# Kernel tuning notes

Hardware: AMD Instinct MI355X
Metric: run time of the kernel (lower is better)

Reference implementation:

```python
import jax, jax.numpy as jnp
import numpy as np

DIM = 1024
HID = 2732  # int(2*4*1024/3) rounded up to multiple of 4
E = 8
TOPK = 2
B, S = 2, 2048


def setup_inputs() -> dict:
    key = jax.random.key(0)
    ks = jax.random.split(key, 5)
    scale = 0.02
    return {
        "x": jax.random.normal(ks[0], (B, S, DIM), dtype=jnp.float32),
        "Wg": jax.random.normal(ks[1], (E, DIM), dtype=jnp.float32) * scale,
        "W1": jax.random.normal(ks[2], (E, HID, DIM), dtype=jnp.float32) * scale,
        "W2": jax.random.normal(ks[3], (E, DIM, HID), dtype=jnp.float32) * scale,
        "W3": jax.random.normal(ks[4], (E, HID, DIM), dtype=jnp.float32) * scale,
    }


def reference(x, Wg, W1, W2, W3):
    b, s, d = x.shape
    xt = x.reshape(b * s, d)                              # [N, d]
    scores = xt @ Wg.T                                    # [N, E]
    w, idx = jax.lax.top_k(scores, TOPK)                  # [N, k]
    w = jax.nn.softmax(w, axis=-1)
    n = xt.shape[0]
    # combine weights scattered back into [N, E] (top-k indices are distinct per row)
    cw = jnp.zeros((n, E), dtype=x.dtype).at[jnp.arange(n)[:, None], idx].set(w)
    # dense per-expert SwiGLU (mathematically identical to masked dispatch)
    h1 = jnp.einsum('nd,ehd->neh', xt, W1)                # [N, E, H]
    h3 = jnp.einsum('nd,ehd->neh', xt, W3)
    h = jax.nn.silu(h1) * h3
    y = jnp.einsum('neh,edh->ned', h, W2)                 # [N, E, d]
    out = jnp.einsum('ned,ne->nd', y, cw)                 # [N, d]
    return out
```

## Files before the change

kernel.cpp:

```cpp
#include <hip/hip_runtime.h>
#include <hip/hip_bf16.h>
#include <stdint.h>

#define DIM   1024
#define HID   2732
#define HPAD  2816
#define NEXP  8
#define NTOK  4096
#define NROW  8192

typedef __attribute__((ext_vector_type(8))) short bf16x8;
typedef __attribute__((ext_vector_type(4))) float f32x4;

__device__ __forceinline__ unsigned short f2bf(float f) {
    union { float f; uint32_t u; } v; v.f = f;
    uint32_t u = v.u;
    return (unsigned short)((u + 0x7FFFu + ((u >> 16) & 1u)) >> 16);
}

#define ASYNC_CP16(g, l) __builtin_amdgcn_global_load_lds( \
    (const __attribute__((address_space(1))) void*)(g), \
    (__attribute__((address_space(3))) void*)(l), 16, 0, 0)

__global__ void conv_w13_kernel(const float* __restrict__ src,
                                unsigned short* __restrict__ dst) {
    size_t t = (size_t)blockIdx.x * 256 + threadIdx.x;
    int d4 = (int)(t & 255);
    size_t rest = t >> 8;
    int hp = (int)(rest % HPAD);
    int e  = (int)(rest / HPAD);
    ushort4 o;
    if (hp < HID) {
        float4 v = *(const float4*)(src + ((size_t)e * HID + hp) * DIM + d4 * 4);
        o.x = f2bf(v.x); o.y = f2bf(v.y); o.z = f2bf(v.z); o.w = f2bf(v.w);
    } else {
        o.x = o.y = o.z = o.w = 0;
    }
    *(ushort4*)(dst + t * 4) = o;
}

__global__ void conv_w2_kernel(const float* __restrict__ src,
                               unsigned short* __restrict__ dst) {
    size_t t = (size_t)blockIdx.x * 256 + threadIdx.x;
    int h4 = (int)(t % (HPAD / 4));
    size_t rest = t / (HPAD / 4);
    int d = (int)(rest % DIM);
    int e = (int)(rest / DIM);
    ushort4 o;
    if (h4 * 4 < HID) {
        float4 v = *(const float4*)(src + ((size_t)e * DIM + d) * HID + h4 * 4);
        o.x = f2bf(v.x); o.y = f2bf(v.y); o.z = f2bf(v.z); o.w = f2bf(v.w);
    } else {
        o.x = o.y = o.z = o.w = 0;
    }
    *(ushort4*)(dst + t * 4) = o;
}

__global__ void route_kernel(const float* __restrict__ x, const float* __restrict__ Wg,
                             int* __restrict__ counts, int* __restrict__ a_exp,
                             int* __restrict__ a_rank, float* __restrict__ a_w) {
    int wave = threadIdx.x >> 6, lane = threadIdx.x & 63;
    int n = blockIdx.x * 4 + wave;
    const float* xr = x + (size_t)n * DIM + lane * 16;
    float p[NEXP];
#pragma unroll
    for (int e = 0; e < NEXP; ++e) p[e] = 0.f;
#pragma unroll
    for (int i = 0; i < 4; ++i) {
        float4 xv = *(const float4*)(xr + i * 4);
#pragma unroll
        for (int e = 0; e < NEXP; ++e) {
            float4 wv = *(const float4*)(Wg + e * DIM + lane * 16 + i * 4);
            p[e] += xv.x * wv.x + xv.y * wv.y + xv.z * wv.z + xv.w * wv.w;
        }
    }
#pragma unroll
    for (int off = 32; off > 0; off >>= 1)
#pragma unroll
        for (int e = 0; e < NEXP; ++e) p[e] += __shfl_xor(p[e], off);
    if (lane == 0) {
        int i1 = -1, i2 = -1; float m1 = -1e30f, m2 = -1e30f;
#pragma unroll
        for (int e = 0; e < NEXP; ++e) {
            float s = p[e];
            if (s > m1) { m2 = m1; i2 = i1; m1 = s; i1 = e; }
            else if (s > m2) { m2 = s; i2 = e; }
        }
        float e2 = __expf(m2 - m1);
        float inv = 1.f / (1.f + e2);
        int a = n * 2;
        a_exp[a] = i1;  a_w[a] = inv;        a_rank[a] = atomicAdd(&counts[i1], 1);
        a_exp[a+1] = i2; a_w[a+1] = e2 * inv; a_rank[a+1] = atomicAdd(&counts[i2], 1);
    }
}

__global__ void scan_kernel(const int* __restrict__ counts, int* __restrict__ offsets) {
    if (threadIdx.x == 0) {
        int s = 0;
        for (int e = 0; e < NEXP; ++e) { offsets[e] = s; s += counts[e]; }
    }
}

__global__ void gather_kernel(const float* __restrict__ x, const int* __restrict__ a_exp,
                              const int* __restrict__ a_rank, const float* __restrict__ a_w,
                              const int* __restrict__ offsets,
                              unsigned short* __restrict__ XG,
                              int* __restrict__ tok_of_row, float* __restrict__ wgt_of_row) {
    int a = blockIdx.x, n = a >> 1;
    int row = offsets[a_exp[a]] + a_rank[a];
    if (threadIdx.x == 0) { tok_of_row[row] = n; wgt_of_row[row] = a_w[a]; }
    float4 xv = *(const float4*)(x + (size_t)n * DIM + threadIdx.x * 4);
    ushort4 o; o.x = f2bf(xv.x); o.y = f2bf(xv.y); o.z = f2bf(xv.z); o.w = f2bf(xv.w);
    *(ushort4*)(XG + (size_t)row * DIM + threadIdx.x * 4) = o;
}

__global__ __launch_bounds__(256, 2) void gemm1_kernel(
    const unsigned short* __restrict__ XG,
    const unsigned short* __restrict__ W1b,
    const unsigned short* __restrict__ W3b,
    const int* __restrict__ counts, const int* __restrict__ offsets,
    unsigned short* __restrict__ Hbuf)
{
    const int e = blockIdx.z, mtile = blockIdx.y, ntile = blockIdx.x;
    const int cnt = counts[e];
    if (mtile * 128 >= cnt) return;
    const int rowstart = offsets[e] + mtile * 128;

    __shared__ __align__(16) unsigned short As[128 * 64];
    __shared__ __align__(16) unsigned short B1s[64 * 64];
    __shared__ __align__(16) unsigned short B3s[64 * 64];

    const int tid = threadIdx.x, lane = tid & 63, wave = tid >> 6;
    const int wm = wave >> 1, wn = wave & 1;
    const int quad = lane >> 4;

    const unsigned short* w1e = W1b + (size_t)e * HPAD * DIM;
    const unsigned short* w3e = W3b + (size_t)e * HPAD * DIM;

    const int srow = tid >> 3, scol = (tid & 7) * 8;
    const unsigned short* ag[4];
#pragma unroll
    for (int r = 0; r < 4; ++r) {
        int grow = rowstart + r * 32 + srow;
        if (grow > NROW - 1) grow = NROW - 1;
        ag[r] = XG + (size_t)grow * DIM + scol;
    }
    const unsigned short* bg1[2]; const unsigned short* bg3[2];
#pragma unroll
    for (int r = 0; r < 2; ++r) {
        int grow = ntile * 64 + r * 32 + srow;
        bg1[r] = w1e + (size_t)grow * DIM + scol;
        bg3[r] = w3e + (size_t)grow * DIM + scol;
    }

    f32x4 acc1[4][2], acc3[4][2];
#pragma unroll
    for (int i = 0; i < 4; ++i)
#pragma unroll
        for (int j = 0; j < 2; ++j) {
            acc1[i][j] = (f32x4){0.f, 0.f, 0.f, 0.f};
            acc3[i][j] = (f32x4){0.f, 0.f, 0.f, 0.f};
        }

    for (int kk = 0; kk < DIM / 64; ++kk) {
        const int k0 = kk * 64;
#pragma unroll
        for (int r = 0; r < 4; ++r)
            ASYNC_CP16(ag[r] + k0, &As[r * 2048 + tid * 8]);
#pragma unroll
        for (int r = 0; r < 2; ++r) {
            ASYNC_CP16(bg1[r] + k0, &B1s[r * 2048 + tid * 8]);
            ASYNC_CP16(bg3[r] + k0, &B3s[r * 2048 + tid * 8]);
        }
        __syncthreads();
#pragma unroll
        for (int ks = 0; ks < 2; ++ks) {
            const int krd = ks * 32 + quad * 8;
            bf16x8 af[4], b1f[2], b3f[2];
#pragma unroll
            for (int i = 0; i < 4; ++i)
                af[i] = *(const bf16x8*)&As[(wm * 64 + i * 16 + (lane & 15)) * 64 + krd];
#pragma unroll
            for (int j = 0; j < 2; ++j) {
                b1f[j] = *(const bf16x8*)&B1s[(wn * 32 + j * 16 + (lane & 15)) * 64 + krd];
                b3f[j] = *(const bf16x8*)&B3s[(wn * 32 + j * 16 + (lane & 15)) * 64 + krd];
            }
#pragma unroll
            for (int i = 0; i < 4; ++i)
#pragma unroll
                for (int j = 0; j < 2; ++j) {
                    acc1[i][j] = __builtin_amdgcn_mfma_f32_16x16x32_bf16(af[i], b1f[j], acc1[i][j], 0, 0, 0);
                    acc3[i][j] = __builtin_amdgcn_mfma_f32_16x16x32_bf16(af[i], b3f[j], acc3[i][j], 0, 0, 0);
                }
        }
        __syncthreads();
    }

    int mvalid = cnt - mtile * 128; if (mvalid > 128) mvalid = 128;
#pragma unroll
    for (int i = 0; i < 4; ++i)
#pragma unroll
        for (int r = 0; r < 4; ++r) {
            int rl = wm * 64 + i * 16 + quad * 4 + r;
            if (rl < mvalid) {
                size_t rowg = (size_t)(rowstart + rl);
#pragma unroll
                for (int j = 0; j < 2; ++j) {
                    float v1 = acc1[i][j][r], v3 = acc3[i][j][r];
                    float s = v1 / (1.f + __expf(-v1));
                    Hbuf[rowg * HPAD + ntile * 64 + wn * 32 + j * 16 + (lane & 15)] = f2bf(s * v3);
                }
            }
        }
}

__global__ __launch_bounds__(256, 2) void gemm2_kernel(
    const unsigned short* __restrict__ Hbuf,
    const unsigned short* __restrict__ W2b,
    const int* __restrict__ counts, const int* __restrict__ offsets,
    const int* __restrict__ tok_of_row, const float* __restrict__ wgt_of_row,
    float* __restrict__ out)
{
    const int e = blockIdx.z, mtile = blockIdx.y, ntile = blockIdx.x;
    const int cnt = counts[e];
    if (mtile * 128 >= cnt) return;
    const int rowstart = offsets[e] + mtile * 128;

    __shared__ __align__(16) unsigned short As[128 * 64];
    __shared__ __align__(16) unsigned short Bs[128 * 64];

    const int tid = threadIdx.x, lane = tid & 63, wave = tid >> 6;
    const int wm = wave >> 1, wn = wave & 1;
    const int quad = lane >> 4;

    const unsigned short* w2e = W2b + (size_t)e * DIM * HPAD;
    const int srow = tid >> 3, scol = (tid & 7) * 8;
    const unsigned short* ag[4]; const unsigned short* bg[4];
#pragma unroll
    for (int r = 0; r < 4; ++r) {
        int grow = rowstart + r * 32 + srow;
        if (grow > NROW - 1) grow = NROW - 1;
        ag[r] = Hbuf + (size_t)grow * HPAD + scol;
        bg[r] = w2e + (size_t)(ntile * 128 + r * 32 + srow) * HPAD + scol;
    }

    f32x4 acc[4][4];
#pragma unroll
    for (int i = 0; i < 4; ++i)
#pragma unroll
        for (int j = 0; j < 4; ++j) acc[i][j] = (f32x4){0.f, 0.f, 0.f, 0.f};

    for (int kk = 0; kk < HPAD / 64; ++kk) {
        const int k0 = kk * 64;
#pragma unroll
        for (int r = 0; r < 4; ++r) {
            ASYNC_CP16(ag[r] + k0, &As[r * 2048 + tid * 8]);
            ASYNC_CP16(bg[r] + k0, &Bs[r * 2048 + tid * 8]);
        }
        __syncthreads();
#pragma unroll
        for (int ks = 0; ks < 2; ++ks) {
            const int krd = ks * 32 + quad * 8;
            bf16x8 af[4], bf[4];
#pragma unroll
            for (int i = 0; i < 4; ++i) {
                af[i] = *(const bf16x8*)&As[(wm * 64 + i * 16 + (lane & 15)) * 64 + krd];
                bf[i] = *(const bf16x8*)&Bs[(wn * 64 + i * 16 + (lane & 15)) * 64 + krd];
            }
#pragma unroll
            for (int i = 0; i < 4; ++i)
#pragma unroll
                for (int j = 0; j < 4; ++j)
                    acc[i][j] = __builtin_amdgcn_mfma_f32_16x16x32_bf16(af[i], bf[j], acc[i][j], 0, 0, 0);
        }
        __syncthreads();
    }

    int mvalid = cnt - mtile * 128; if (mvalid > 128) mvalid = 128;
#pragma unroll
    for (int i = 0; i < 4; ++i)
#pragma unroll
        for (int r = 0; r < 4; ++r) {
            int rl = wm * 64 + i * 16 + quad * 4 + r;
            if (rl < mvalid) {
                int rowg = rowstart + rl;
                int tok = tok_of_row[rowg];
                float wt = wgt_of_row[rowg];
                float* orow = out + (size_t)tok * DIM + ntile * 128 + wn * 64 + (lane & 15);
#pragma unroll
                for (int j = 0; j < 4; ++j)
                    atomicAdd(orow + j * 16, acc[i][j][r] * wt);
            }
        }
}

extern "C" void kernel_launch(void* const* d_in, const int* in_sizes, int n_in,
                              void* d_out, int out_size, void* d_ws, size_t ws_size,
                              hipStream_t stream) {
    const float* x  = (const float*)d_in[0];
    const float* Wg = (const float*)d_in[1];
    const float* W1 = (const float*)d_in[2];
    const float* W2 = (const float*)d_in[3];
    const float* W3 = (const float*)d_in[4];
    float* out = (float*)d_out;

    char* ws = (char*)d_ws;
    size_t off = 0;
    auto alloc = [&](size_t bytes) -> void* {
        void* p = ws + off;
        off = (off + bytes + 255) & ~(size_t)255;
        return p;
    };
    int*   counts      = (int*)alloc(NEXP * 4);
    int*   offsets     = (int*)alloc(NEXP * 4);
    int*   a_exp       = (int*)alloc(NROW * 4);
    int*   a_rank      = (int*)alloc(NROW * 4);
    float* a_w         = (float*)alloc(NROW * 4);
    int*   tok_of_row  = (int*)alloc(NROW * 4);
    float* wgt_of_row  = (float*)alloc(NROW * 4);
    unsigned short* XG   = (unsigned short*)alloc((size_t)NROW * DIM * 2);
    unsigned short* Hbuf = (unsigned short*)alloc((size_t)NROW * HPAD * 2);
    unsigned short* W1b  = (unsigned short*)alloc((size_t)NEXP * HPAD * DIM * 2);
    unsigned short* W3b  = (unsigned short*)alloc((size_t)NEXP * HPAD * DIM * 2);
    unsigned short* W2b  = (unsigned short*)alloc((size_t)NEXP * DIM * HPAD * 2);

    hipMemsetAsync(counts, 0, NEXP * 4, stream);
    hipMemsetAsync(out, 0, (size_t)out_size * 4, stream);

    const int convBlocks = (NEXP * HPAD * DIM / 4) / 256;
    conv_w13_kernel<<<convBlocks, 256, 0, stream>>>(W1, W1b);
    conv_w13_kernel<<<convBlocks, 256, 0, stream>>>(W3, W3b);
    conv_w2_kernel<<<convBlocks, 256, 0, stream>>>(W2, W2b);

    route_kernel<<<NTOK / 4, 256, 0, stream>>>(x, Wg, counts, a_exp, a_rank, a_w);
    scan_kernel<<<1, 64, 0, stream>>>(counts, offsets);
    gather_kernel<<<NROW, 256, 0, stream>>>(x, a_exp, a_rank, a_w, offsets,
                                            XG, tok_of_row, wgt_of_row);

    gemm1_kernel<<<dim3(HPAD / 64, 32, NEXP), 256, 0, stream>>>(
        XG, W1b, W3b, counts, offsets, Hbuf);
    gemm2_kernel<<<dim3(DIM / 128, 32, NEXP), 256, 0, stream>>>(
        Hbuf, W2b, counts, offsets, tok_of_row, wgt_of_row, out);
}
```

Baseline: 642.7 us.

## Swizzle LDS tiles and replace atomic scatter with per-row buffer plus combine kernel

XOR-swizzles the 16-byte column chunks of the shared-memory A/B tiles in both GEMMs, on the async global-to-LDS copy and on the MFMA fragment reads, to reduce LDS bank conflicts. gemm2 now writes unweighted expert outputs to a per-row fp32 buffer that reuses the W1b workspace after gemm1 has finished. A new combine kernel applies the two routing weights and sums per token, which removes the float atomics and the memset of the output. The m-tile grid grows to 64 so that experts with more than 4096 assigned rows are fully covered. The cost is an extra write and read of an 8192x1024 fp32 buffer and one more launch.

Measured after the change: 597.4 us. 1.08x faster.

```diff
diff --git a/kernel.cpp b/kernel.cpp
--- a/kernel.cpp
+++ b/kernel.cpp
@@ -102,13 +102,13 @@
 }
 
 __global__ void gather_kernel(const float* __restrict__ x, const int* __restrict__ a_exp,
-                              const int* __restrict__ a_rank, const float* __restrict__ a_w,
+                              const int* __restrict__ a_rank,
                               const int* __restrict__ offsets,
                               unsigned short* __restrict__ XG,
-                              int* __restrict__ tok_of_row, float* __restrict__ wgt_of_row) {
+                              int* __restrict__ row_of_a) {
     int a = blockIdx.x, n = a >> 1;
     int row = offsets[a_exp[a]] + a_rank[a];
-    if (threadIdx.x == 0) { tok_of_row[row] = n; wgt_of_row[row] = a_w[a]; }
+    if (threadIdx.x == 0) row_of_a[a] = row;
     float4 xv = *(const float4*)(x + (size_t)n * DIM + threadIdx.x * 4);
     ushort4 o; o.x = f2bf(xv.x); o.y = f2bf(xv.y); o.z = f2bf(xv.z); o.w = f2bf(xv.w);
     *(ushort4*)(XG + (size_t)row * DIM + threadIdx.x * 4) = o;
@@ -137,7 +137,8 @@
     const unsigned short* w1e = W1b + (size_t)e * HPAD * DIM;
     const unsigned short* w3e = W3b + (size_t)e * HPAD * DIM;
 
-    const int srow = tid >> 3, scol = (tid & 7) * 8;
+    const int srow = tid >> 3;
+    const int scol = (((tid & 7) ^ (srow & 7)) * 8);
     const unsigned short* ag[4];
 #pragma unroll
     for (int r = 0; r < 4; ++r) {
@@ -175,15 +176,18 @@
         __syncthreads();
 #pragma unroll
         for (int ks = 0; ks < 2; ++ks) {
-            const int krd = ks * 32 + quad * 8;
+            const int cbase = ks * 4 + quad;
             bf16x8 af[4], b1f[2], b3f[2];
 #pragma unroll
-            for (int i = 0; i < 4; ++i)
-                af[i] = *(const bf16x8*)&As[(wm * 64 + i * 16 + (lane & 15)) * 64 + krd];
+            for (int i = 0; i < 4; ++i) {
+                int rl = wm * 64 + i * 16 + (lane & 15);
+                af[i] = *(const bf16x8*)&As[rl * 64 + ((cbase ^ (rl & 7)) * 8)];
+            }
 #pragma unroll
             for (int j = 0; j < 2; ++j) {
-                b1f[j] = *(const bf16x8*)&B1s[(wn * 32 + j * 16 + (lane & 15)) * 64 + krd];
-                b3f[j] = *(const bf16x8*)&B3s[(wn * 32 + j * 16 + (lane & 15)) * 64 + krd];
+                int rl1 = wn * 32 + j * 16 + (lane & 15);
+                b1f[j] = *(const bf16x8*)&B1s[rl1 * 64 + ((cbase ^ (rl1 & 7)) * 8)];
+                b3f[j] = *(const bf16x8*)&B3s[rl1 * 64 + ((cbase ^ (rl1 & 7)) * 8)];
             }
 #pragma unroll
             for (int i = 0; i < 4; ++i)
@@ -218,8 +222,7 @@
     const unsigned short* __restrict__ Hbuf,
     const unsigned short* __restrict__ W2b,
     const int* __restrict__ counts, const int* __restrict__ offsets,
-    const int* __restrict__ tok_of_row, const float* __restrict__ wgt_of_row,
-    float* __restrict__ out)
+    float* __restrict__ Ybuf)
 {
     const int e = blockIdx.z, mtile = blockIdx.y, ntile = blockIdx.x;
     const int cnt = counts[e];
@@ -234,7 +237,8 @@
     const int quad = lane >> 4;
 
     const unsigned short* w2e = W2b + (size_t)e * DIM * HPAD;
-    const int srow = tid >> 3, scol = (tid & 7) * 8;
+    const int srow = tid >> 3;
+    const int scol = (((tid & 7) ^ (srow & 7)) * 8);
     const unsigned short* ag[4]; const unsigned short* bg[4];
 #pragma unroll
     for (int r = 0; r < 4; ++r) {
@@ -260,12 +264,14 @@
         __syncthreads();
 #pragma unroll
         for (int ks = 0; ks < 2; ++ks) {
-            const int krd = ks * 32 + quad * 8;
+            const int cbase = ks * 4 + quad;
             bf16x8 af[4], bf[4];
 #pragma unroll
             for (int i = 0; i < 4; ++i) {
-                af[i] = *(const bf16x8*)&As[(wm * 64 + i * 16 + (lane & 15)) * 64 + krd];
-                bf[i] = *(const bf16x8*)&Bs[(wn * 64 + i * 16 + (lane & 15)) * 64 + krd];
+                int rla = wm * 64 + i * 16 + (lane & 15);
+                int rlb = wn * 64 + i * 16 + (lane & 15);
+                af[i] = *(const bf16x8*)&As[rla * 64 + ((cbase ^ (rla & 7)) * 8)];
+                bf[i] = *(const bf16x8*)&Bs[rlb * 64 + ((cbase ^ (rlb & 7)) * 8)];
             }
 #pragma unroll
             for (int i = 0; i < 4; ++i)
@@ -284,14 +290,29 @@
             int rl = wm * 64 + i * 16 + quad * 4 + r;
             if (rl < mvalid) {
                 int rowg = rowstart + rl;
-                int tok = tok_of_row[rowg];
-                float wt = wgt_of_row[rowg];
-                float* orow = out + (size_t)tok * DIM + ntile * 128 + wn * 64 + (lane & 15);
+                float* yrow = Ybuf + (size_t)rowg * DIM + ntile * 128 + wn * 64 + (lane & 15);
 #pragma unroll
                 for (int j = 0; j < 4; ++j)
-                    atomicAdd(orow + j * 16, acc[i][j][r] * wt);
-            }
-        }
+                    yrow[j * 16] = acc[i][j][r];
+            }
+        }
+}
+
+__global__ void combine_kernel(const float* __restrict__ Ybuf,
+                               const int* __restrict__ row_of_a,
+                               const float* __restrict__ a_w,
+                               float* __restrict__ out) {
+    int n = blockIdx.x, t = threadIdx.x;
+    int r0 = row_of_a[2 * n], r1 = row_of_a[2 * n + 1];
+    float w0 = a_w[2 * n], w1 = a_w[2 * n + 1];
+    float4 y0 = *(const float4*)(Ybuf + (size_t)r0 * DIM + t * 4);
+    float4 y1 = *(const float4*)(Ybuf + (size_t)r1 * DIM + t * 4);
+    float4 o;
+    o.x = w0 * y0.x + w1 * y1.x;
+    o.y = w0 * y0.y + w1 * y1.y;
+    o.z = w0 * y0.z + w1 * y1.z;
+    o.w = w0 * y0.w + w1 * y1.w;
+    *(float4*)(out + (size_t)n * DIM + t * 4) = o;
 }
 
 extern "C" void kernel_launch(void* const* d_in, const int* in_sizes, int n_in,
@@ -316,16 +337,15 @@
     int*   a_exp       = (int*)alloc(NROW * 4);
     int*   a_rank      = (int*)alloc(NROW * 4);
     float* a_w         = (float*)alloc(NROW * 4);
-    int*   tok_of_row  = (int*)alloc(NROW * 4);
-    float* wgt_of_row  = (float*)alloc(NROW * 4);
+    int*   row_of_a    = (int*)alloc(NROW * 4);
     unsigned short* XG   = (unsigned short*)alloc((size_t)NROW * DIM * 2);
     unsigned short* Hbuf = (unsigned short*)alloc((size_t)NROW * HPAD * 2);
     unsigned short* W1b  = (unsigned short*)alloc((size_t)NEXP * HPAD * DIM * 2);
     unsigned short* W3b  = (unsigned short*)alloc((size_t)NEXP * HPAD * DIM * 2);
     unsigned short* W2b  = (unsigned short*)alloc((size_t)NEXP * DIM * HPAD * 2);
+    float* Ybuf = (float*)W1b;
 
     hipMemsetAsync(counts, 0, NEXP * 4, stream);
-    hipMemsetAsync(out, 0, (size_t)out_size * 4, stream);
 
     const int convBlocks = (NEXP * HPAD * DIM / 4) / 256;
     conv_w13_kernel<<<convBlocks, 256, 0, stream>>>(W1, W1b);
@@ -334,11 +354,11 @@
 
     route_kernel<<<NTOK / 4, 256, 0, stream>>>(x, Wg, counts, a_exp, a_rank, a_w);
     scan_kernel<<<1, 64, 0, stream>>>(counts, offsets);
-    gather_kernel<<<NROW, 256, 0, stream>>>(x, a_exp, a_rank, a_w, offsets,
-                                            XG, tok_of_row, wgt_of_row);
-
-    gemm1_kernel<<<dim3(HPAD / 64, 32, NEXP), 256, 0, stream>>>(
+    gather_kernel<<<NROW, 256, 0, stream>>>(x, a_exp, a_rank, offsets, XG, row_of_a);
+
+    gemm1_kernel<<<dim3(HPAD / 64, 64, NEXP), 256, 0, stream>>>(
         XG, W1b, W3b, counts, offsets, Hbuf);
-    gemm2_kernel<<<dim3(DIM / 128, 32, NEXP), 256, 0, stream>>>(
-        Hbuf, W2b, counts, offsets, tok_of_row, wgt_of_row, out);
-}
+    gemm2_kernel<<<dim3(DIM / 128, 64, NEXP), 256, 0, stream>>>(
+        Hbuf, W2b, counts, offsets, Ybuf);
+    combine_kernel<<<NTOK, 256, 0, stream>>>(Ybuf, row_of_a, a_w, out);
+}
```
